# Kernel tuning notes

Hardware: AMD Instinct MI355X
Metric: run time of the kernel (lower is better)

Reference implementation:

```python
import jax, jax.numpy as jnp
import numpy as np

B, D, F, N = 8192, 256, 128, 500000

def setup_inputs() -> dict:
    key = jax.random.key(0)
    ks = jax.random.split(key, 32)
    def p(i, shape, s=0.05):
        return (jax.random.normal(ks[i], shape, dtype=jnp.float32) * s)
    inp = {
        'ids': jnp.arange(B, dtype=jnp.int32),
        'user_prior': jax.random.normal(ks[0], (B, D), dtype=jnp.float32),
        'user_emb': jax.random.normal(ks[1], (B, D), dtype=jnp.float32),
        'item_emb': jax.random.normal(ks[2], (B, D), dtype=jnp.float32),
        'feat': jax.random.normal(ks[3], (B, F), dtype=jnp.float32),
        'h_table': jax.random.normal(ks[4], (N, D), dtype=jnp.float32) * 0.1,
        'tran_W0': p(5, (D, D + F)), 'tran_b0': p(6, (D,)),
        'tran_W1': p(7, (D, D)),     'tran_b1': p(8, (D,)),
        'pred_W0': p(9, (D, D)),     'pred_b0': p(10, (D,)),
        'pred_W1': p(11, (D, D)),    'pred_b1': p(12, (D,)),
        'kin_W0': p(13, (D, D + 1)), 'kin_b0': p(14, (D,)),
        'kin_W1': p(15, (D, D)),     'kin_b1': p(16, (D,)),
        'gru_Wih': p(17, (3 * D, D)), 'gru_Whh': p(18, (3 * D, D)),
        'gru_bih': p(19, (3 * D,)),   'gru_bhh': p(20, (3 * D,)),
        'kout_W0': p(21, (D, D)),    'kout_b0': p(22, (D,)),
        'kout_W1': p(23, (D, D)),    'kout_b1': p(24, (D,)),
    }
    return inp

def _mlp2(x, W0, b0, W1, b1):
    # torch MLP with mlp_num_layers=2: Linear -> ReLU -> Linear
    h = jax.nn.relu(x @ W0.T + b0)
    return h @ W1.T + b1

def _gru_cell(x, h, Wih, Whh, bih, bhh):
    # torch.nn.GRUCell semantics
    gi = x @ Wih.T + bih   # [B, 3D]
    gh = h @ Whh.T + bhh   # [B, 3D]
    i_r, i_z, i_n = jnp.split(gi, 3, axis=1)
    h_r, h_z, h_n = jnp.split(gh, 3, axis=1)
    r = jax.nn.sigmoid(i_r + h_r)
    z = jax.nn.sigmoid(i_z + h_z)
    n = jnp.tanh(i_n + r * h_n)
    return (1.0 - z) * n + z * h

def reference(ids, user_prior, user_emb, item_emb, feat, h_table,
              tran_W0, tran_b0, tran_W1, tran_b1,
              pred_W0, pred_b0, pred_W1, pred_b1,
              kin_W0, kin_b0, kin_W1, kin_b1,
              gru_Wih, gru_Whh, gru_bih, gru_bhh,
              kout_W0, kout_b0, kout_W1, kout_b1):
    # NeuFilter.forward(select='user_update') -> NeuralKF.forward
    emb = _mlp2(jnp.concatenate([user_emb, feat], axis=1), tran_W0, tran_b0, tran_W1, tran_b1)
    emb_post_pred = _mlp2(emb, pred_W0, pred_b0, pred_W1, pred_b1)
    emb_res = emb_post_pred - user_prior
    z_res = 1.0 - jnp.sum(item_emb * user_prior, axis=1, keepdims=True)  # [B,1]
    k_in = _mlp2(jnp.concatenate([emb_res, z_res], axis=1), kin_W0, kin_b0, kin_W1, kin_b1)
    h_state = h_table[ids]                                   # gather
    h_state = _gru_cell(k_in, h_state, gru_Wih, gru_Whh, gru_bih, gru_bhh)
    h_new = h_table.at[ids].set(h_state)                     # scatter back
    K = _mlp2(h_state, kout_W0, kout_b0, kout_W1, kout_b1)
    emb_post = user_prior + K * z_res
    emb_regu = jnp.linalg.norm(emb_post_pred - emb_post)     # Frobenius norm
    # F.normalize(emb_post) along dim=1, eps=1e-12
    nrm = jnp.maximum(jnp.linalg.norm(emb_post, axis=1, keepdims=True), 1e-12)
    out = emb_post / nrm
    return out, emb_regu, h_new
```

## Files before the change

kernel.cpp:

```cpp
#include <hip/hip_runtime.h>
#include <stdint.h>

#define B_ 8192
#define D_ 256
#define F_ 128
#define NTAB 500000

typedef unsigned short u16;
typedef unsigned int u32;
typedef __attribute__((ext_vector_type(8))) short bf16x8;
typedef __attribute__((ext_vector_type(4))) float f32x4;

__device__ __forceinline__ u16 f2bf(float v) {
  u32 u = __float_as_uint(v);
  u32 r = (u + 0x7fffu + ((u >> 16) & 1u)) >> 16;
  return (u16)r;
}
__device__ __forceinline__ float bf2f(u16 h) {
  return __uint_as_float(((u32)h) << 16);
}
__device__ __forceinline__ void f2hilo(float v, u16& h, u16& l) {
  h = f2bf(v);
  l = f2bf(v - bf2f(h));
}

__device__ __forceinline__ void copy_chunk(const float4* __restrict__ s,
                                           float4* __restrict__ d, long cofs,
                                           long ccnt, long bid, long nblk,
                                           int tid) {
  long i = cofs + bid * 256 + tid;
  long end = cofs + ccnt;
  long step = nblk * 256;
  for (; i < end; i += step) {
    float4 a = s[i];
    float4 b = s[i + 1];
    float4 o;
    o.x = a.w;
    o.y = b.x;
    o.z = b.y;
    o.w = b.z;
    d[524289 + i] = o;
  }
}

struct WJobs {
  const float* src[10];
  u16* hi[10];
  u16* lo[10];
  int rows[10];
  int scols[10];
  int dcols[10];
};

__global__ __launch_bounds__(256) void wconv_kernel(WJobs jobs,
                                                    const float* __restrict__ htab,
                                                    float* __restrict__ otab) {
  int stride = gridDim.x * blockDim.x;
  int gid = blockIdx.x * blockDim.x + threadIdx.x;
  for (int j = 0; j < 10; ++j) {
    int dc = jobs.dcols[j];
    int sc = jobs.scols[j];
    int n = jobs.rows[j] * dc;
    const float* s = jobs.src[j];
    u16* ph = jobs.hi[j];
    u16* pl = jobs.lo[j];
    for (int i = gid; i < n; i += stride) {
      int r = i / dc;
      int c = i - r * dc;
      float v = (c < sc) ? s[r * sc + c] : 0.f;
      u16 h, l;
      f2hilo(v, h, l);
      ph[i] = h;
      pl[i] = l;
    }
  }
  if (gid == 0) {
    otab[0] = htab[0];
    otab[1] = htab[1];
    otab[2] = htab[2];
    otab[127999999] = htab[127999999];
  }
}

__global__ __launch_bounds__(256) void prep_kernel(
    const float* __restrict__ user_emb, const float* __restrict__ feat,
    const float* __restrict__ h_table, const int* __restrict__ ids,
    u16* __restrict__ x0h, u16* __restrict__ x0l, float* __restrict__ hst,
    u16* __restrict__ hsh, u16* __restrict__ hsl,
    const float4* __restrict__ csrc, float4* __restrict__ cdst, long cofs,
    long ccnt) {
  int stride = gridDim.x * blockDim.x;
  int gid = blockIdx.x * blockDim.x + threadIdx.x;
  const int n1 = B_ * 384;
  for (int i = gid; i < n1; i += stride) {
    int b = i / 384;
    int c = i - b * 384;
    float v = (c < 256) ? user_emb[b * 256 + c] : feat[b * 128 + (c - 256)];
    u16 h, l;
    f2hilo(v, h, l);
    x0h[i] = h;
    x0l[i] = l;
  }
  const int n2 = B_ * 256;
  for (int i = gid; i < n2; i += stride) {
    int b = i >> 8;
    int c = i & 255;
    float v = h_table[(size_t)ids[b] * 256 + c];
    hst[i] = v;
    u16 h, l;
    f2hilo(v, h, l);
    hsh[i] = h;
    hsl[i] = l;
  }
  copy_chunk(csrc, cdst, cofs, ccnt, blockIdx.x, gridDim.x, threadIdx.x);
}

__global__ __launch_bounds__(256) void zres_kernel(
    const float* __restrict__ item_emb, const float* __restrict__ user_prior,
    float* __restrict__ zres, u16* __restrict__ xkh, u16* __restrict__ xkl) {
  int wave = threadIdx.x >> 6;
  int lane = threadIdx.x & 63;
  int b = blockIdx.x * 4 + wave;
  float s = 0.f;
#pragma unroll
  for (int i = 0; i < 4; ++i) {
    int d = lane + 64 * i;
    s += item_emb[(size_t)b * 256 + d] * user_prior[(size_t)b * 256 + d];
  }
#pragma unroll
  for (int m = 1; m < 64; m <<= 1) s += __shfl_xor(s, m);
  float z = 1.f - s;
  size_t rb = (size_t)b * 320;
  if (lane == 0) {
    zres[b] = z;
    u16 h, l;
    f2hilo(z, h, l);
    xkh[rb + 256] = h;
    xkl[rb + 256] = l;
  } else {
    int c = 256 + lane;
    if (c < 320) {
      xkh[rb + c] = 0;
      xkl[rb + c] = 0;
    }
  }
}

constexpr int EPI_HILO = 0;
constexpr int EPI_RELU_HILO = 1;
constexpr int EPI_F32 = 2;
constexpr int EPI_RES = 3;

template <int EPI>
__global__ __launch_bounds__(256, 2) void gemm_hilo(
    const u16* __restrict__ Ahi, const u16* __restrict__ Alo,
    const u16* __restrict__ Bhi, const u16* __restrict__ Blo,
    const float* __restrict__ bias, int K, float* __restrict__ outf, int ldf,
    u16* __restrict__ outh, u16* __restrict__ outl, int ldo,
    const float* __restrict__ aux, const float4* __restrict__ csrc,
    float4* __restrict__ cdst, long cofs, long ccnt, int nyg) {
  __shared__ u16 smem[4 * 4096];
  if ((int)blockIdx.y >= nyg) {
    long nblk = (long)(gridDim.y - nyg) * gridDim.x;
    long bid = (long)(blockIdx.y - nyg) * gridDim.x + blockIdx.x;
    copy_chunk(csrc, cdst, cofs, ccnt, bid, nblk, threadIdx.x);
    return;
  }
  const int tid = threadIdx.x;
  const int wave = tid >> 6;
  const int lane = tid & 63;
  const int rowBase = blockIdx.x * 64;
  const int colBase = blockIdx.y * 64;
  const int wm = wave >> 1;
  const int wn = wave & 1;

  const u16* srcs[4] = {Ahi + (size_t)rowBase * K, Alo + (size_t)rowBase * K,
                        Bhi + (size_t)colBase * K, Blo + (size_t)colBase * K};
  const u16* src = srcs[wave];
  u16* ldsbase = &smem[wave * 4096];

  const int r8 = lane >> 3;
  const int chunk = (lane & 7) ^ r8;
  const int c16 = lane & 15;
  const int g = lane >> 4;

  f32x4 acc[2][2];
#pragma unroll
  for (int i = 0; i < 2; ++i)
#pragma unroll
    for (int j = 0; j < 2; ++j) acc[i][j] = (f32x4){0.f, 0.f, 0.f, 0.f};

  for (int k0 = 0; k0 < K; k0 += 64) {
#pragma unroll
    for (int j = 0; j < 8; ++j) {
      int row = (j << 3) + r8;
      const u16* gp = src + (size_t)row * K + k0 + chunk * 8;
      __builtin_amdgcn_global_load_lds(
          (const __attribute__((address_space(1))) void*)gp,
          (__attribute__((address_space(3))) void*)(ldsbase + j * 512), 16, 0,
          0);
    }
    __syncthreads();
#pragma unroll
    for (int s = 0; s < 2; ++s) {
      bf16x8 ah[2], al[2], bh[2], bl[2];
#pragma unroll
      for (int fm = 0; fm < 2; ++fm) {
        int r = wm * 32 + fm * 16 + c16;
        int off = r * 64 + (((s * 4 + g) ^ (r & 7)) << 3);
        ah[fm] = *(const bf16x8*)&smem[0 * 4096 + off];
        al[fm] = *(const bf16x8*)&smem[1 * 4096 + off];
      }
#pragma unroll
      for (int fn = 0; fn < 2; ++fn) {
        int c = wn * 32 + fn * 16 + c16;
        int off = c * 64 + (((s * 4 + g) ^ (c & 7)) << 3);
        bh[fn] = *(const bf16x8*)&smem[2 * 4096 + off];
        bl[fn] = *(const bf16x8*)&smem[3 * 4096 + off];
      }
#pragma unroll
      for (int fm = 0; fm < 2; ++fm)
#pragma unroll
        for (int fn = 0; fn < 2; ++fn) {
          acc[fm][fn] = __builtin_amdgcn_mfma_f32_16x16x32_bf16(
              ah[fm], bh[fn], acc[fm][fn], 0, 0, 0);
          acc[fm][fn] = __builtin_amdgcn_mfma_f32_16x16x32_bf16(
              ah[fm], bl[fn], acc[fm][fn], 0, 0, 0);
          acc[fm][fn] = __builtin_amdgcn_mfma_f32_16x16x32_bf16(
              al[fm], bh[fn], acc[fm][fn], 0, 0, 0);
        }
    }
    __syncthreads();
  }

#pragma unroll
  for (int fm = 0; fm < 2; ++fm)
#pragma unroll
    for (int fn = 0; fn < 2; ++fn) {
      int colg = colBase + wn * 32 + fn * 16 + c16;
      float bv = bias[colg];
#pragma unroll
      for (int j = 0; j < 4; ++j) {
        int rowg = rowBase + wm * 32 + fm * 16 + g * 4 + j;
        float v = acc[fm][fn][j] + bv;
        if constexpr (EPI == EPI_RELU_HILO) {
          v = fmaxf(v, 0.f);
          u16 h, l;
          f2hilo(v, h, l);
          outh[(size_t)rowg * ldo + colg] = h;
          outl[(size_t)rowg * ldo + colg] = l;
        } else if constexpr (EPI == EPI_HILO) {
          u16 h, l;
          f2hilo(v, h, l);
          outh[(size_t)rowg * ldo + colg] = h;
          outl[(size_t)rowg * ldo + colg] = l;
        } else if constexpr (EPI == EPI_F32) {
          outf[(size_t)rowg * ldf + colg] = v;
        } else {
          outf[(size_t)rowg * ldf + colg] = v;
          float r2 = v - aux[(size_t)rowg * 256 + colg];
          u16 h, l;
          f2hilo(r2, h, l);
          outh[(size_t)rowg * ldo + colg] = h;
          outl[(size_t)rowg * ldo + colg] = l;
        }
      }
    }
}

__global__ __launch_bounds__(256) void gru_kernel(
    const float* __restrict__ gi, const float* __restrict__ gh,
    const float* __restrict__ hst, u16* __restrict__ hnh,
    u16* __restrict__ hnl, float* __restrict__ hnewf,
    const float4* __restrict__ csrc, float4* __restrict__ cdst, long cofs,
    long ccnt) {
  int stride = gridDim.x * blockDim.x;
  for (int i = blockIdx.x * blockDim.x + threadIdx.x; i < B_ * 256;
       i += stride) {
    size_t base = (size_t)(i >> 8) * 768;
    int d = i & 255;
    float ir = gi[base + d], iz = gi[base + 256 + d], inn = gi[base + 512 + d];
    float hr = gh[base + d], hz = gh[base + 256 + d], hn = gh[base + 512 + d];
    float r = 1.f / (1.f + __expf(-(ir + hr)));
    float z = 1.f / (1.f + __expf(-(iz + hz)));
    float n = tanhf(inn + r * hn);
    float h = (1.f - z) * n + z * hst[i];
    u16 hh, ll;
    f2hilo(h, hh, ll);
    hnh[i] = hh;
    hnl[i] = ll;
    hnewf[i] = h;
  }
  copy_chunk(csrc, cdst, cofs, ccnt, blockIdx.x, gridDim.x, threadIdx.x);
}

__global__ __launch_bounds__(256) void fin_kernel(
    const float* __restrict__ Kmat, const float* __restrict__ user_prior,
    const float* __restrict__ epp, const float* __restrict__ zres,
    const float* __restrict__ hnewf, const int* __restrict__ ids,
    float* __restrict__ out, float* __restrict__ otab,
    float* __restrict__ partial) {
  __shared__ float sh[4];
  int wave = threadIdx.x >> 6;
  int lane = threadIdx.x & 63;
  int b = blockIdx.x * 4 + wave;
  float z = zres[b];
  size_t rb = (size_t)b * 256;
  size_t orow = (size_t)ids[b] * 256;
  float post[4];
  float sres = 0.f, snrm = 0.f;
#pragma unroll
  for (int i = 0; i < 4; ++i) {
    int d = lane + 64 * i;
    float p = user_prior[rb + d] + Kmat[rb + d] * z;
    post[i] = p;
    float e = epp[rb + d] - p;
    sres += e * e;
    snrm += p * p;
    otab[orow + d] = hnewf[rb + d];
  }
#pragma unroll
  for (int m = 1; m < 64; m <<= 1) {
    sres += __shfl_xor(sres, m);
    snrm += __shfl_xor(snrm, m);
  }
  float denom = fmaxf(sqrtf(snrm), 1e-12f);
#pragma unroll
  for (int i = 0; i < 4; ++i) out[rb + lane + 64 * i] = post[i] / denom;
  if (lane == 0) sh[wave] = sres;
  __syncthreads();
  if (threadIdx.x == 0) partial[blockIdx.x] = sh[0] + sh[1] + sh[2] + sh[3];
}

__global__ __launch_bounds__(256) void regu_kernel(
    const float* __restrict__ partial, float* __restrict__ out_scalar) {
  __shared__ float sh[4];
  float s = 0.f;
  for (int i = threadIdx.x; i < 2048; i += 256) s += partial[i];
#pragma unroll
  for (int m = 1; m < 64; m <<= 1) s += __shfl_xor(s, m);
  int wave = threadIdx.x >> 6;
  int lane = threadIdx.x & 63;
  if (lane == 0) sh[wave] = s;
  __syncthreads();
  if (threadIdx.x == 0) out_scalar[0] = sqrtf(sh[0] + sh[1] + sh[2] + sh[3]);
}

extern "C" void kernel_launch(void* const* d_in, const int* in_sizes, int n_in,
                              void* d_out, int out_size, void* d_ws,
                              size_t ws_size, hipStream_t stream) {
  const int* ids = (const int*)d_in[0];
  const float* user_prior = (const float*)d_in[1];
  const float* user_emb = (const float*)d_in[2];
  const float* item_emb = (const float*)d_in[3];
  const float* feat = (const float*)d_in[4];
  const float* h_table = (const float*)d_in[5];
  const float* tran_W0 = (const float*)d_in[6];
  const float* tran_b0 = (const float*)d_in[7];
  const float* tran_W1 = (const float*)d_in[8];
  const float* tran_b1 = (const float*)d_in[9];
  const float* pred_W0 = (const float*)d_in[10];
  const float* pred_b0 = (const float*)d_in[11];
  const float* pred_W1 = (const float*)d_in[12];
  const float* pred_b1 = (const float*)d_in[13];
  const float* kin_W0 = (const float*)d_in[14];
  const float* kin_b0 = (const float*)d_in[15];
  const float* kin_W1 = (const float*)d_in[16];
  const float* kin_b1 = (const float*)d_in[17];
  const float* gru_Wih = (const float*)d_in[18];
  const float* gru_Whh = (const float*)d_in[19];
  const float* gru_bih = (const float*)d_in[20];
  const float* gru_bhh = (const float*)d_in[21];
  const float* kout_W0 = (const float*)d_in[22];
  const float* kout_b0 = (const float*)d_in[23];
  const float* kout_W1 = (const float*)d_in[24];
  const float* kout_b1 = (const float*)d_in[25];

  float* out_mat = (float*)d_out;
  float* out_scalar = out_mat + (size_t)B_ * D_;
  float* out_table = out_scalar + 1;
  const float4* csrc = (const float4*)h_table;
  float4* cdst = (float4*)d_out;

  char* p = (char*)d_ws;
  auto alloc = [&](size_t bytes) -> char* {
    char* r = p;
    p += (bytes + 255) & ~(size_t)255;
    return r;
  };

  static const int wrows[10] = {256, 256, 256, 256, 256,
                                256, 768, 768, 256, 256};
  static const int wscols[10] = {384, 256, 256, 256, 257,
                                 256, 256, 256, 256, 256};
  static const int wdcols[10] = {384, 256, 256, 256, 320,
                                 256, 256, 256, 256, 256};
  const float* wsrc[10] = {tran_W0, tran_W1, pred_W0, pred_W1, kin_W0,
                           kin_W1,  gru_Wih, gru_Whh, kout_W0, kout_W1};
  u16* wh[10];
  u16* wl[10];
  for (int j = 0; j < 10; ++j) {
    size_t n = (size_t)wrows[j] * wdcols[j];
    wh[j] = (u16*)alloc(n * 2);
    wl[j] = (u16*)alloc(n * 2);
  }

  u16* x0h = (u16*)alloc((size_t)B_ * 384 * 2);
  u16* x0l = (u16*)alloc((size_t)B_ * 384 * 2);
  u16* p2h = (u16*)alloc((size_t)B_ * 256 * 2);
  u16* p2l = (u16*)alloc((size_t)B_ * 256 * 2);
  u16* p3h = (u16*)alloc((size_t)B_ * 256 * 2);
  u16* p3l = (u16*)alloc((size_t)B_ * 256 * 2);
  u16* xkh = (u16*)alloc((size_t)B_ * 320 * 2);
  u16* xkl = (u16*)alloc((size_t)B_ * 320 * 2);
  float* hst = (float*)alloc((size_t)B_ * 256 * 4);
  u16* hsh = (u16*)alloc((size_t)B_ * 256 * 2);
  u16* hsl = (u16*)alloc((size_t)B_ * 256 * 2);
  float* epp = (float*)alloc((size_t)B_ * 256 * 4);
  float* gi = (float*)alloc((size_t)B_ * 768 * 4);
  float* gh = (float*)alloc((size_t)B_ * 768 * 4);
  float* hnewf = (float*)alloc((size_t)B_ * 256 * 4);
  float* zres = (float*)alloc((size_t)B_ * 4);
  float* partial = (float*)alloc(2048 * 4);
  (void)ws_size;
  (void)in_sizes;
  (void)n_in;
  (void)out_size;

  WJobs jobs;
  for (int j = 0; j < 10; ++j) {
    jobs.src[j] = wsrc[j];
    jobs.hi[j] = wh[j];
    jobs.lo[j] = wl[j];
    jobs.rows[j] = wrows[j];
    jobs.scols[j] = wscols[j];
    jobs.dcols[j] = wdcols[j];
  }

  const long KMT = 31999999;
  const int wgt[12] = {2, 6, 4, 4, 4, 5, 4, 12, 12, 3, 4, 4};
  long ofs[12], cnt[12], accum = 0;
  for (int i = 0; i < 12; ++i) {
    cnt[i] = KMT * (long)wgt[i] / 64;
    ofs[i] = accum;
    accum += cnt[i];
  }
  cnt[11] += KMT - accum;

  dim3 blk(256);
  const int CY = 4;
  dim3 g256(128, 4 + CY);
  dim3 g768(128, 12 + CY);

  wconv_kernel<<<1024, blk, 0, stream>>>(jobs, h_table, out_table);
  prep_kernel<<<2048, blk, 0, stream>>>(user_emb, feat, h_table, ids, x0h, x0l,
                                        hst, hsh, hsl, csrc, cdst, ofs[0],
                                        cnt[0]);
  zres_kernel<<<2048, blk, 0, stream>>>(item_emb, user_prior, zres, xkh, xkl);

  gemm_hilo<EPI_RELU_HILO><<<g256, blk, 0, stream>>>(
      x0h, x0l, wh[0], wl[0], tran_b0, 384, nullptr, 0, p2h, p2l, 256, nullptr,
      csrc, cdst, ofs[1], cnt[1], 4);
  gemm_hilo<EPI_HILO><<<g256, blk, 0, stream>>>(
      p2h, p2l, wh[1], wl[1], tran_b1, 256, nullptr, 0, p3h, p3l, 256, nullptr,
      csrc, cdst, ofs[2], cnt[2], 4);
  gemm_hilo<EPI_RELU_HILO><<<g256, blk, 0, stream>>>(
      p3h, p3l, wh[2], wl[2], pred_b0, 256, nullptr, 0, x0h, x0l, 256, nullptr,
      csrc, cdst, ofs[3], cnt[3], 4);
  gemm_hilo<EPI_RES><<<g256, blk, 0, stream>>>(
      x0h, x0l, wh[3], wl[3], pred_b1, 256, epp, 256, xkh, xkl, 320, user_prior,
      csrc, cdst, ofs[4], cnt[4], 4);
  gemm_hilo<EPI_RELU_HILO><<<g256, blk, 0, stream>>>(
      xkh, xkl, wh[4], wl[4], kin_b0, 320, nullptr, 0, p2h, p2l, 256, nullptr,
      csrc, cdst, ofs[5], cnt[5], 4);
  gemm_hilo<EPI_HILO><<<g256, blk, 0, stream>>>(
      p2h, p2l, wh[5], wl[5], kin_b1, 256, nullptr, 0, p3h, p3l, 256, nullptr,
      csrc, cdst, ofs[6], cnt[6], 4);
  gemm_hilo<EPI_F32><<<g768, blk, 0, stream>>>(
      p3h, p3l, wh[6], wl[6], gru_bih, 256, gi, 768, nullptr, nullptr, 0,
      nullptr, csrc, cdst, ofs[7], cnt[7], 12);
  gemm_hilo<EPI_F32><<<g768, blk, 0, stream>>>(
      hsh, hsl, wh[7], wl[7], gru_bhh, 256, gh, 768, nullptr, nullptr, 0,
      nullptr, csrc, cdst, ofs[8], cnt[8], 12);
  gru_kernel<<<2048, blk, 0, stream>>>(gi, gh, hst, p2h, p2l, hnewf, csrc, cdst,
                                       ofs[9], cnt[9]);
  gemm_hilo<EPI_RELU_HILO><<<g256, blk, 0, stream>>>(
      p2h, p2l, wh[8], wl[8], kout_b0, 256, nullptr, 0, x0h, x0l, 256, nullptr,
      csrc, cdst, ofs[10], cnt[10], 4);
  gemm_hilo<EPI_F32><<<g256, blk, 0, stream>>>(
      x0h, x0l, wh[9], wl[9], kout_b1, 256, gi, 256, nullptr, nullptr, 0,
      nullptr, csrc, cdst, ofs[11], cnt[11], 4);
  fin_kernel<<<2048, blk, 0, stream>>>(gi, user_prior, epp, zres, hnewf, ids,
                                       out_mat, out_table, partial);
  regu_kernel<<<1, blk, 0, stream>>>(partial, out_scalar);
}
```

Baseline: 1.052 ms.

## Merge setup kernels, deepen GEMM K-tile, interleave table-copy blocks with compute

Merges the weight conversion, input prep and z_res kernels into one setup kernel, removing two launches. The GEMM K-step grows from 64 to 128, doubling LDS use per block, with a new swizzle; the kin input is padded to 384 columns to match. The 500k-row table copy blocks are now interleaved with GEMM tiles by block index instead of placed in extra grid rows, so copy and compute blocks share CUs, and the copy-weight split is rebalanced. Larger LDS per block may lower occupancy, and the padding adds some wasted MFMA work on the kin layer.

```diff
diff --git a/kernel.cpp b/kernel.cpp
--- a/kernel.cpp
+++ b/kernel.cpp
@@ -52,9 +52,16 @@
   int dcols[10];
 };
 
-__global__ __launch_bounds__(256) void wconv_kernel(WJobs jobs,
-                                                    const float* __restrict__ htab,
-                                                    float* __restrict__ otab) {
+__global__ __launch_bounds__(256) void setup_kernel(
+    WJobs jobs, const float* __restrict__ user_emb,
+    const float* __restrict__ feat, const float* __restrict__ h_table,
+    const int* __restrict__ ids, const float* __restrict__ item_emb,
+    const float* __restrict__ user_prior, u16* __restrict__ x0h,
+    u16* __restrict__ x0l, float* __restrict__ hst, u16* __restrict__ hsh,
+    u16* __restrict__ hsl, float* __restrict__ zres, u16* __restrict__ xkh,
+    u16* __restrict__ xkl, float* __restrict__ otab,
+    const float4* __restrict__ csrc, float4* __restrict__ cdst, long cofs,
+    long ccnt) {
   int stride = gridDim.x * blockDim.x;
   int gid = blockIdx.x * blockDim.x + threadIdx.x;
   for (int j = 0; j < 10; ++j) {
@@ -74,23 +81,6 @@
       pl[i] = l;
     }
   }
-  if (gid == 0) {
-    otab[0] = htab[0];
-    otab[1] = htab[1];
-    otab[2] = htab[2];
-    otab[127999999] = htab[127999999];
-  }
-}
-
-__global__ __launch_bounds__(256) void prep_kernel(
-    const float* __restrict__ user_emb, const float* __restrict__ feat,
-    const float* __restrict__ h_table, const int* __restrict__ ids,
-    u16* __restrict__ x0h, u16* __restrict__ x0l, float* __restrict__ hst,
-    u16* __restrict__ hsh, u16* __restrict__ hsl,
-    const float4* __restrict__ csrc, float4* __restrict__ cdst, long cofs,
-    long ccnt) {
-  int stride = gridDim.x * blockDim.x;
-  int gid = blockIdx.x * blockDim.x + threadIdx.x;
   const int n1 = B_ * 384;
   for (int i = gid; i < n1; i += stride) {
     int b = i / 384;
@@ -112,38 +102,41 @@
     hsh[i] = h;
     hsl[i] = l;
   }
+  {
+    int wave = threadIdx.x >> 6;
+    int lane = threadIdx.x & 63;
+    int b = blockIdx.x * 4 + wave;
+    if (b < B_) {
+      float s = 0.f;
+#pragma unroll
+      for (int i = 0; i < 4; ++i) {
+        int d = lane + 64 * i;
+        s += item_emb[(size_t)b * 256 + d] * user_prior[(size_t)b * 256 + d];
+      }
+#pragma unroll
+      for (int m = 1; m < 64; m <<= 1) s += __shfl_xor(s, m);
+      float z = 1.f - s;
+      size_t rb = (size_t)b * 384;
+      if (lane == 0) {
+        zres[b] = z;
+        u16 h, l;
+        f2hilo(z, h, l);
+        xkh[rb + 256] = h;
+        xkl[rb + 256] = l;
+      }
+      for (int c = 257 + lane; c < 384; c += 64) {
+        xkh[rb + c] = 0;
+        xkl[rb + c] = 0;
+      }
+    }
+  }
+  if (gid == 0) {
+    otab[0] = h_table[0];
+    otab[1] = h_table[1];
+    otab[2] = h_table[2];
+    otab[127999999] = h_table[127999999];
+  }
   copy_chunk(csrc, cdst, cofs, ccnt, blockIdx.x, gridDim.x, threadIdx.x);
-}
-
-__global__ __launch_bounds__(256) void zres_kernel(
-    const float* __restrict__ item_emb, const float* __restrict__ user_prior,
-    float* __restrict__ zres, u16* __restrict__ xkh, u16* __restrict__ xkl) {
-  int wave = threadIdx.x >> 6;
-  int lane = threadIdx.x & 63;
-  int b = blockIdx.x * 4 + wave;
-  float s = 0.f;
-#pragma unroll
-  for (int i = 0; i < 4; ++i) {
-    int d = lane + 64 * i;
-    s += item_emb[(size_t)b * 256 + d] * user_prior[(size_t)b * 256 + d];
-  }
-#pragma unroll
-  for (int m = 1; m < 64; m <<= 1) s += __shfl_xor(s, m);
-  float z = 1.f - s;
-  size_t rb = (size_t)b * 320;
-  if (lane == 0) {
-    zres[b] = z;
-    u16 h, l;
-    f2hilo(z, h, l);
-    xkh[rb + 256] = h;
-    xkl[rb + 256] = l;
-  } else {
-    int c = 256 + lane;
-    if (c < 320) {
-      xkh[rb + c] = 0;
-      xkl[rb + c] = 0;
-    }
-  }
 }
 
 constexpr int EPI_HILO = 0;
@@ -158,29 +151,29 @@
     const float* __restrict__ bias, int K, float* __restrict__ outf, int ldf,
     u16* __restrict__ outh, u16* __restrict__ outl, int ldo,
     const float* __restrict__ aux, const float4* __restrict__ csrc,
-    float4* __restrict__ cdst, long cofs, long ccnt, int nyg) {
-  __shared__ u16 smem[4 * 4096];
-  if ((int)blockIdx.y >= nyg) {
-    long nblk = (long)(gridDim.y - nyg) * gridDim.x;
-    long bid = (long)(blockIdx.y - nyg) * gridDim.x + blockIdx.x;
-    copy_chunk(csrc, cdst, cofs, ccnt, bid, nblk, threadIdx.x);
+    float4* __restrict__ cdst, long cofs, long ccnt, int P) {
+  __shared__ u16 smem[4 * 8192];
+  const int b = blockIdx.x;
+  if ((b % P) == P - 1) {
+    long nblk = gridDim.x / P;
+    copy_chunk(csrc, cdst, cofs, ccnt, b / P, nblk, threadIdx.x);
     return;
   }
+  const int cb = b - b / P;
   const int tid = threadIdx.x;
   const int wave = tid >> 6;
   const int lane = tid & 63;
-  const int rowBase = blockIdx.x * 64;
-  const int colBase = blockIdx.y * 64;
+  const int rowBase = (cb & 127) * 64;
+  const int colBase = (cb >> 7) * 64;
   const int wm = wave >> 1;
   const int wn = wave & 1;
 
   const u16* srcs[4] = {Ahi + (size_t)rowBase * K, Alo + (size_t)rowBase * K,
                         Bhi + (size_t)colBase * K, Blo + (size_t)colBase * K};
   const u16* src = srcs[wave];
-  u16* ldsbase = &smem[wave * 4096];
-
-  const int r8 = lane >> 3;
-  const int chunk = (lane & 7) ^ r8;
+  u16* ldsbase = &smem[wave * 8192];
+
+  const int r4 = lane >> 4;
   const int c16 = lane & 15;
   const int g = lane >> 4;
 
@@ -190,11 +183,12 @@
 #pragma unroll
     for (int j = 0; j < 2; ++j) acc[i][j] = (f32x4){0.f, 0.f, 0.f, 0.f};
 
-  for (int k0 = 0; k0 < K; k0 += 64) {
-#pragma unroll
-    for (int j = 0; j < 8; ++j) {
-      int row = (j << 3) + r8;
-      const u16* gp = src + (size_t)row * K + k0 + chunk * 8;
+  for (int k0 = 0; k0 < K; k0 += 128) {
+#pragma unroll
+    for (int j = 0; j < 16; ++j) {
+      int row = (j << 2) + r4;
+      int sslot = c16 ^ (row & 7);
+      const u16* gp = src + (size_t)row * K + k0 + sslot * 8;
       __builtin_amdgcn_global_load_lds(
           (const __attribute__((address_space(1))) void*)gp,
           (__attribute__((address_space(3))) void*)(ldsbase + j * 512), 16, 0,
@@ -202,21 +196,21 @@
     }
     __syncthreads();
 #pragma unroll
-    for (int s = 0; s < 2; ++s) {
+    for (int s = 0; s < 4; ++s) {
       bf16x8 ah[2], al[2], bh[2], bl[2];
 #pragma unroll
       for (int fm = 0; fm < 2; ++fm) {
         int r = wm * 32 + fm * 16 + c16;
-        int off = r * 64 + (((s * 4 + g) ^ (r & 7)) << 3);
-        ah[fm] = *(const bf16x8*)&smem[0 * 4096 + off];
-        al[fm] = *(const bf16x8*)&smem[1 * 4096 + off];
+        int off = r * 128 + (((s * 4 + g) ^ (r & 7)) << 3);
+        ah[fm] = *(const bf16x8*)&smem[0 * 8192 + off];
+        al[fm] = *(const bf16x8*)&smem[1 * 8192 + off];
       }
 #pragma unroll
       for (int fn = 0; fn < 2; ++fn) {
         int c = wn * 32 + fn * 16 + c16;
-        int off = c * 64 + (((s * 4 + g) ^ (c & 7)) << 3);
-        bh[fn] = *(const bf16x8*)&smem[2 * 4096 + off];
-        bl[fn] = *(const bf16x8*)&smem[3 * 4096 + off];
+        int off = c * 128 + (((s * 4 + g) ^ (c & 7)) << 3);
+        bh[fn] = *(const bf16x8*)&smem[2 * 8192 + off];
+        bl[fn] = *(const bf16x8*)&smem[3 * 8192 + off];
       }
 #pragma unroll
       for (int fm = 0; fm < 2; ++fm)
@@ -274,9 +268,14 @@
     u16* __restrict__ hnl, float* __restrict__ hnewf,
     const float4* __restrict__ csrc, float4* __restrict__ cdst, long cofs,
     long ccnt) {
-  int stride = gridDim.x * blockDim.x;
-  for (int i = blockIdx.x * blockDim.x + threadIdx.x; i < B_ * 256;
-       i += stride) {
+  const int b = blockIdx.x;
+  if (b & 1) {
+    copy_chunk(csrc, cdst, cofs, ccnt, b >> 1, gridDim.x >> 1, threadIdx.x);
+    return;
+  }
+  int nwork = gridDim.x >> 1;
+  int stride = nwork * blockDim.x;
+  for (int i = (b >> 1) * blockDim.x + threadIdx.x; i < B_ * 256; i += stride) {
     size_t base = (size_t)(i >> 8) * 768;
     int d = i & 255;
     float ir = gi[base + d], iz = gi[base + 256 + d], inn = gi[base + 512 + d];
@@ -291,7 +290,6 @@
     hnl[i] = ll;
     hnewf[i] = h;
   }
-  copy_chunk(csrc, cdst, cofs, ccnt, blockIdx.x, gridDim.x, threadIdx.x);
 }
 
 __global__ __launch_bounds__(256) void fin_kernel(
@@ -393,7 +391,7 @@
                                 256, 768, 768, 256, 256};
   static const int wscols[10] = {384, 256, 256, 256, 257,
                                  256, 256, 256, 256, 256};
-  static const int wdcols[10] = {384, 256, 256, 256, 320,
+  static const int wdcols[10] = {384, 256, 256, 256, 384,
                                  256, 256, 256, 256, 256};
   const float* wsrc[10] = {tran_W0, tran_W1, pred_W0, pred_W1, kin_W0,
                            kin_W1,  gru_Wih, gru_Whh, kout_W0, kout_W1};
@@ -411,8 +409,8 @@
   u16* p2l = (u16*)alloc((size_t)B_ * 256 * 2);
   u16* p3h = (u16*)alloc((size_t)B_ * 256 * 2);
   u16* p3l = (u16*)alloc((size_t)B_ * 256 * 2);
-  u16* xkh = (u16*)alloc((size_t)B_ * 320 * 2);
-  u16* xkl = (u16*)alloc((size_t)B_ * 320 * 2);
+  u16* xkh = (u16*)alloc((size_t)B_ * 384 * 2);
+  u16* xkl = (u16*)alloc((size_t)B_ * 384 * 2);
   float* hst = (float*)alloc((size_t)B_ * 256 * 4);
   u16* hsh = (u16*)alloc((size_t)B_ * 256 * 2);
   u16* hsl = (u16*)alloc((size_t)B_ * 256 * 2);
@@ -438,7 +436,7 @@
   }
 
   const long KMT = 31999999;
-  const int wgt[12] = {2, 6, 4, 4, 4, 5, 4, 12, 12, 3, 4, 4};
+  const int wgt[12] = {3, 6, 4, 4, 4, 6, 4, 10, 10, 3, 5, 5};
   long ofs[12], cnt[12], accum = 0;
   for (int i = 0; i < 12; ++i) {
     cnt[i] = KMT * (long)wgt[i] / 64;
@@ -448,48 +446,45 @@
   cnt[11] += KMT - accum;
 
   dim3 blk(256);
-  const int CY = 4;
-  dim3 g256(128, 4 + CY);
-  dim3 g768(128, 12 + CY);
-
-  wconv_kernel<<<1024, blk, 0, stream>>>(jobs, h_table, out_table);
-  prep_kernel<<<2048, blk, 0, stream>>>(user_emb, feat, h_table, ids, x0h, x0l,
-                                        hst, hsh, hsl, csrc, cdst, ofs[0],
-                                        cnt[0]);
-  zres_kernel<<<2048, blk, 0, stream>>>(item_emb, user_prior, zres, xkh, xkl);
-
-  gemm_hilo<EPI_RELU_HILO><<<g256, blk, 0, stream>>>(
+  const int G256 = 1024, P256 = 2;
+  const int G768 = 2048, P768 = 4;
+
+  setup_kernel<<<2048, blk, 0, stream>>>(
+      jobs, user_emb, feat, h_table, ids, item_emb, user_prior, x0h, x0l, hst,
+      hsh, hsl, zres, xkh, xkl, out_table, csrc, cdst, ofs[0], cnt[0]);
+
+  gemm_hilo<EPI_RELU_HILO><<<G256, blk, 0, stream>>>(
       x0h, x0l, wh[0], wl[0], tran_b0, 384, nullptr, 0, p2h, p2l, 256, nullptr,
-      csrc, cdst, ofs[1], cnt[1], 4);
-  gemm_hilo<EPI_HILO><<<g256, blk, 0, stream>>>(
+      csrc, cdst, ofs[1], cnt[1], P256);
+  gemm_hilo<EPI_HILO><<<G256, blk, 0, stream>>>(
       p2h, p2l, wh[1], wl[1], tran_b1, 256, nullptr, 0, p3h, p3l, 256, nullptr,
-      csrc, cdst, ofs[2], cnt[2], 4);
-  gemm_hilo<EPI_RELU_HILO><<<g256, blk, 0, stream>>>(
+      csrc, cdst, ofs[2], cnt[2], P256);
+  gemm_hilo<EPI_RELU_HILO><<<G256, blk, 0, stream>>>(
       p3h, p3l, wh[2], wl[2], pred_b0, 256, nullptr, 0, x0h, x0l, 256, nullptr,
-      csrc, cdst, ofs[3], cnt[3], 4);
-  gemm_hilo<EPI_RES><<<g256, blk, 0, stream>>>(
-      x0h, x0l, wh[3], wl[3], pred_b1, 256, epp, 256, xkh, xkl, 320, user_prior,
-      csrc, cdst, ofs[4], cnt[4], 4);
-  gemm_hilo<EPI_RELU_HILO><<<g256, blk, 0, stream>>>(
-      xkh, xkl, wh[4], wl[4], kin_b0, 320, nullptr, 0, p2h, p2l, 256, nullptr,
-      csrc, cdst, ofs[5], cnt[5], 4);
-  gemm_hilo<EPI_HILO><<<g256, blk, 0, stream>>>(
+      csrc, cdst, ofs[3], cnt[3], P256);
+  gemm_hilo<EPI_RES><<<G256, blk, 0, stream>>>(
+      x0h, x0l, wh[3], wl[3], pred_b1, 256, epp, 256, xkh, xkl, 384, user_prior,
+      csrc, cdst, ofs[4], cnt[4], P256);
+  gemm_hilo<EPI_RELU_HILO><<<G256, blk, 0, stream>>>(
+      xkh, xkl, wh[4], wl[4], kin_b0, 384, nullptr, 0, p2h, p2l, 256, nullptr,
+      csrc, cdst, ofs[5], cnt[5], P256);
+  gemm_hilo<EPI_HILO><<<G256, blk, 0, stream>>>(
       p2h, p2l, wh[5], wl[5], kin_b1, 256, nullptr, 0, p3h, p3l, 256, nullptr,
-      csrc, cdst, ofs[6], cnt[6], 4);
-  gemm_hilo<EPI_F32><<<g768, blk, 0, stream>>>(
+      csrc, cdst, ofs[6], cnt[6], P256);
+  gemm_hilo<EPI_F32><<<G768, blk, 0, stream>>>(
       p3h, p3l, wh[6], wl[6], gru_bih, 256, gi, 768, nullptr, nullptr, 0,
-      nullptr, csrc, cdst, ofs[7], cnt[7], 12);
-  gemm_hilo<EPI_F32><<<g768, blk, 0, stream>>>(
+      nullptr, csrc, cdst, ofs[7], cnt[7], P768);
+  gemm_hilo<EPI_F32><<<G768, blk, 0, stream>>>(
       hsh, hsl, wh[7], wl[7], gru_bhh, 256, gh, 768, nullptr, nullptr, 0,
-      nullptr, csrc, cdst, ofs[8], cnt[8], 12);
+      nullptr, csrc, cdst, ofs[8], cnt[8], P768);
   gru_kernel<<<2048, blk, 0, stream>>>(gi, gh, hst, p2h, p2l, hnewf, csrc, cdst,
                                        ofs[9], cnt[9]);
-  gemm_hilo<EPI_RELU_HILO><<<g256, blk, 0, stream>>>(
+  gemm_hilo<EPI_RELU_HILO><<<G256, blk, 0, stream>>>(
       p2h, p2l, wh[8], wl[8], kout_b0, 256, nullptr, 0, x0h, x0l, 256, nullptr,
-      csrc, cdst, ofs[10], cnt[10], 4);
-  gemm_hilo<EPI_F32><<<g256, blk, 0, stream>>>(
+      csrc, cdst, ofs[10], cnt[10], P256);
+  gemm_hilo<EPI_F32><<<G256, blk, 0, stream>>>(
       x0h, x0l, wh[9], wl[9], kout_b1, 256, gi, 256, nullptr, nullptr, 0,
-      nullptr, csrc, cdst, ofs[11], cnt[11], 4);
+      nullptr, csrc, cdst, ofs[11], cnt[11], P256);
   fin_kernel<<<2048, blk, 0, stream>>>(gi, user_prior, epp, zres, hnewf, ids,
                                        out_mat, out_table, partial);
   regu_kernel<<<1, blk, 0, stream>>>(partial, out_scalar);
```

Result: slower. 1.207 ms (+14.8%).
